# Optimization experiments

Hardware: AMD Instinct MI355X
Metric: run time of the kernel (lower is better)

The kernel has to match this reference:

```python
import jax, jax.numpy as jnp
import numpy as np

EPS = 1e-5
SLOPE = 0.01  # torch LeakyReLU default negative_slope


def _stage(h, W):
    # h: [B, N, k, Cin]; W: [Cout, Cin] (1x1 conv, no bias)
    h = jnp.einsum('bnkc,oc->bnko', h, W)
    # InstanceNorm2d (affine=False): normalize per (batch, channel) over spatial (N, k)
    mean = jnp.mean(h, axis=(1, 2), keepdims=True)
    var = jnp.var(h, axis=(1, 2), keepdims=True)
    h = (h - mean) * jax.lax.rsqrt(var + EPS)
    return jnp.where(h >= 0, h, SLOPE * h)


def setup_inputs() -> dict:
    key = jax.random.key(0)
    k1, k2, k3, k4, k5 = jax.random.split(key, 5)
    B, N, D, K, C = 8, 4096, 64, 20, 64
    x = jax.random.normal(k1, (B, N, D), dtype=jnp.float32)
    ind = jax.random.randint(k2, (B, N, K), 0, B * N, dtype=jnp.int64)
    W1 = jax.random.normal(k3, (C, 2 * D), dtype=jnp.float32) * 0.05
    W2 = jax.random.normal(k4, (C, C), dtype=jnp.float32) * 0.05
    W3 = jax.random.normal(k5, (C, C), dtype=jnp.float32) * 0.05
    return {"x": x, "ind": ind, "W1": W1, "W2": W2, "W3": W3}


def reference(x, ind, W1, W2, W3):
    B, N, D = x.shape
    k = ind.shape[2]
    # Gather neighbors via global (B*N) indices, as in the torch code
    y = x.reshape(B * N, D)[ind.reshape(B * N, k)].reshape(B, N, k, D)  # [B,N,k,D]
    xe = jnp.broadcast_to(x[:, :, None, :], (B, N, k, D))
    feat = jnp.concatenate([y - xe, xe], axis=3)  # [B,N,k,2D]
    h = _stage(feat, W1)
    h = _stage(h, W2)
    h = _stage(h, W3)
    # max-pool over k neighbors -> [B, N, Cout]
    return jnp.max(h, axis=2)
```

## Files before the change

kernel.cpp:

```cpp
#include <hip/hip_runtime.h>

#define BDIM 8
#define NPTS 4096
#define KNEI 20
#define BN (BDIM*NPTS)
#define NKCNT (NPTS*KNEI)
#define EPSI 1e-5f
#define SLOPE 0.01f

typedef _Float16 half_t;
typedef __attribute__((ext_vector_type(2))) _Float16 h2v;
typedef __attribute__((ext_vector_type(4))) _Float16 h4v;
typedef __attribute__((ext_vector_type(8))) _Float16 h8v;
typedef __attribute__((ext_vector_type(4))) float f32x4;
typedef __attribute__((ext_vector_type(2))) float f32x2;

__device__ __forceinline__ unsigned long long pack4_f16(const f32x4& a) {
    unsigned p0 = __builtin_bit_cast(unsigned, __builtin_amdgcn_cvt_pkrtz(a[0], a[1]));
    unsigned p1 = __builtin_bit_cast(unsigned, __builtin_amdgcn_cvt_pkrtz(a[2], a[3]));
    return ((unsigned long long)p1 << 32) | p0;
}

__global__ __launch_bounds__(256) void k0_uv(const float* __restrict__ x,
        const float* __restrict__ W1, const float* __restrict__ W2,
        const float* __restrict__ W3, half_t* __restrict__ u,
        half_t* __restrict__ v, half_t* __restrict__ Wh2,
        half_t* __restrict__ Wh3) {
    int tid = threadIdx.x;
    if (blockIdx.x >= BN / 16) {
        const float* src = (blockIdx.x == BN / 16) ? W2 : W3;
        half_t* dst = (blockIdx.x == BN / 16) ? Wh2 : Wh3;
        for (int i = tid; i < 4096; i += 256) dst[i] = (half_t)src[i];
        return;
    }
    __shared__ float wlds[64 * 129];
    __shared__ float xs[16 * 64];
    int m0 = blockIdx.x * 16;
    for (int i = tid; i < 8192; i += 256)
        wlds[(i >> 7) * 129 + (i & 127)] = W1[i];
    for (int i = tid; i < 1024; i += 256)
        xs[i] = x[m0 * 64 + i];
    __syncthreads();
    int o = tid & 63;
    int r0 = tid >> 6;
    float au[4] = {0.f, 0.f, 0.f, 0.f};
    float av[4] = {0.f, 0.f, 0.f, 0.f};
    for (int c = 0; c < 64; ++c) {
        float wa = wlds[o * 129 + c];
        float wb = wlds[o * 129 + 64 + c];
        float wd = wb - wa;
#pragma unroll
        for (int jj = 0; jj < 4; ++jj) {
            float xv = xs[(r0 + jj * 4) * 64 + c];
            au[jj] += xv * wa;
            av[jj] += xv * wd;
        }
    }
#pragma unroll
    for (int jj = 0; jj < 4; ++jj) {
        int m = m0 + r0 + jj * 4;
        u[(size_t)m * 64 + o] = (half_t)au[jj];
        v[(size_t)m * 64 + o] = (half_t)av[jj];
    }
}

__global__ __launch_bounds__(256) void k1_stats1(const half_t* __restrict__ u,
        const half_t* __restrict__ v, const int* __restrict__ ind,
        float* __restrict__ s1) {
    __shared__ float sacc[128];
    int tid = threadIdx.x;
    if (tid < 128) sacc[tid] = 0.f;
    int lane = tid & 63, w = tid >> 6;
    int b = blockIdx.x >> 8;
    int n0 = (blockIdx.x & 255) << 4;
    int p = b * NPTS + n0 + w * 4 + (lane >> 4);
    int c4 = lane & 15;
    h4v vv = *(const h4v*)(v + (size_t)p * 64 + c4 * 4);
    const int* ip = ind + (size_t)p * 20;
    float s0 = 0, s1v = 0, s2v = 0, s3v = 0, q0 = 0, q1 = 0, q2 = 0, q3 = 0;
#pragma unroll
    for (int r = 0; r < 20; ++r) {
        int idx = ip[r];
        h4v uu = *(const h4v*)(u + (size_t)idx * 64 + c4 * 4);
        h4v h = uu + vv;
        float f0 = h[0], f1 = h[1], f2 = h[2], f3 = h[3];
        s0 += f0; q0 = fmaf(f0, f0, q0);
        s1v += f1; q1 = fmaf(f1, f1, q1);
        s2v += f2; q2 = fmaf(f2, f2, q2);
        s3v += f3; q3 = fmaf(f3, f3, q3);
    }
    __syncthreads();
    atomicAdd(&sacc[c4 * 4 + 0], s0);  atomicAdd(&sacc[c4 * 4 + 1], s1v);
    atomicAdd(&sacc[c4 * 4 + 2], s2v); atomicAdd(&sacc[c4 * 4 + 3], s3v);
    atomicAdd(&sacc[64 + c4 * 4 + 0], q0); atomicAdd(&sacc[64 + c4 * 4 + 1], q1);
    atomicAdd(&sacc[64 + c4 * 4 + 2], q2); atomicAdd(&sacc[64 + c4 * 4 + 3], q3);
    __syncthreads();
    if (tid < 128)
        atomicAdd(&s1[(tid >> 6) * 512 + b * 64 + (tid & 63)], sacc[tid]);
}

__global__ __launch_bounds__(256, 3) void k2_stats2(const half_t* __restrict__ u,
        const half_t* __restrict__ v, const int* __restrict__ ind,
        const half_t* __restrict__ Wh2, const float* __restrict__ s1,
        float* __restrict__ s2) {
    __shared__ float sacc[128];
    int tid = threadIdx.x;
    if (tid < 128) sacc[tid] = 0.f;
    int lane = tid & 63, w = tid >> 6;
    int l15 = lane & 15, q = lane >> 4;
    int b = blockIdx.x >> 8;
    int n0 = (blockIdx.x & 255) << 4;
    int base = b * NPTS + n0;
    h8v aw[4][2];
#pragma unroll
    for (int mt = 0; mt < 4; ++mt)
#pragma unroll
        for (int kc = 0; kc < 2; ++kc)
            aw[mt][kc] = *(const h8v*)(Wh2 + (mt * 16 + l15) * 64 + kc * 32 + q * 8);
    const float inv = 1.0f / (float)NKCNT;
    h8v r1v[2], m1v[2];
#pragma unroll
    for (int kc = 0; kc < 2; ++kc)
#pragma unroll
        for (int j = 0; j < 8; ++j) {
            int c = kc * 32 + q * 8 + j;
            float mm = s1[b * 64 + c] * inv;
            float va = s1[512 + b * 64 + c] * inv - mm * mm;
            float rs = rsqrtf(va + EPSI);
            r1v[kc][j] = (half_t)rs;
            m1v[kc][j] = (half_t)(-mm * rs);
        }
    int idxs[5];
#pragma unroll
    for (int nt = 0; nt < 5; ++nt)
        idxs[nt] = ind[(size_t)base * 20 + w * 80 + nt * 16 + l15];
    float ss[4][4] = {}, sq[4][4] = {};
#pragma unroll
    for (int nt = 0; nt < 5; ++nt) {
        int row = w * 80 + nt * 16 + l15;
        int p = (row * 3277) >> 16;
        const half_t* up = u + (size_t)idxs[nt] * 64;
        const half_t* vp = v + (size_t)(base + p) * 64;
        h8v bfr[2];
#pragma unroll
        for (int kc = 0; kc < 2; ++kc) {
            h8v uu = *(const h8v*)(up + kc * 32 + q * 8);
            h8v vvv = *(const h8v*)(vp + kc * 32 + q * 8);
            h8v h = uu + vvv;
            h8v t = h * r1v[kc] + m1v[kc];
            bfr[kc] = __builtin_elementwise_max(t, t * (half_t)SLOPE);
        }
#pragma unroll
        for (int mt = 0; mt < 4; ++mt) {
            f32x4 a = {0.f, 0.f, 0.f, 0.f};
            a = __builtin_amdgcn_mfma_f32_16x16x32_f16(aw[mt][0], bfr[0], a, 0, 0, 0);
            a = __builtin_amdgcn_mfma_f32_16x16x32_f16(aw[mt][1], bfr[1], a, 0, 0, 0);
#pragma unroll
            for (int j = 0; j < 4; ++j) {
                ss[mt][j] += a[j];
                sq[mt][j] = fmaf(a[j], a[j], sq[mt][j]);
            }
        }
    }
#pragma unroll
    for (int m = 1; m < 16; m <<= 1)
#pragma unroll
        for (int mt = 0; mt < 4; ++mt)
#pragma unroll
            for (int j = 0; j < 4; ++j) {
                ss[mt][j] += __shfl_xor(ss[mt][j], m, 64);
                sq[mt][j] += __shfl_xor(sq[mt][j], m, 64);
            }
    __syncthreads();
    if (l15 == 0) {
#pragma unroll
        for (int mt = 0; mt < 4; ++mt)
#pragma unroll
            for (int j = 0; j < 4; ++j) {
                atomicAdd(&sacc[mt * 16 + q * 4 + j], ss[mt][j]);
                atomicAdd(&sacc[64 + mt * 16 + q * 4 + j], sq[mt][j]);
            }
    }
    __syncthreads();
    if (tid < 128)
        atomicAdd(&s2[(tid >> 6) * 512 + b * 64 + (tid & 63)], sacc[tid]);
}

__global__ __launch_bounds__(256, 3) void k3_fused(const half_t* __restrict__ u,
        const half_t* __restrict__ v, const int* __restrict__ ind,
        const half_t* __restrict__ Wh2, const half_t* __restrict__ Wh3,
        const float* __restrict__ s1, const float* __restrict__ s2,
        float* __restrict__ s3, float* __restrict__ out) {
    __shared__ __align__(16) unsigned char tile[40960];
    __shared__ float sacc[128];
    int tid = threadIdx.x;
    if (tid < 128) sacc[tid] = 0.f;
    int lane = tid & 63, w = tid >> 6;
    int l15 = lane & 15, q = lane >> 4;
    int b = blockIdx.x >> 8;
    int n0 = (blockIdx.x & 255) << 4;
    int base = b * NPTS + n0;
    const float inv = 1.0f / (float)NKCNT;
    h8v r1v[2], m1v[2], r2v[2], m2v[2];
#pragma unroll
    for (int kc = 0; kc < 2; ++kc)
#pragma unroll
        for (int j = 0; j < 8; ++j) {
            int c = kc * 32 + q * 8 + j;
            float mm = s1[b * 64 + c] * inv;
            float va = s1[512 + b * 64 + c] * inv - mm * mm;
            float rs = rsqrtf(va + EPSI);
            r1v[kc][j] = (half_t)rs;
            m1v[kc][j] = (half_t)(-mm * rs);
            float mm2 = s2[b * 64 + c] * inv;
            float va2 = s2[512 + b * 64 + c] * inv - mm2 * mm2;
            float rs2 = rsqrtf(va2 + EPSI);
            r2v[kc][j] = (half_t)rs2;
            m2v[kc][j] = (half_t)(-mm2 * rs2);
        }
    h8v aw[4][2];
#pragma unroll
    for (int mt = 0; mt < 4; ++mt)
#pragma unroll
        for (int kc = 0; kc < 2; ++kc)
            aw[mt][kc] = *(const h8v*)(Wh2 + (mt * 16 + l15) * 64 + kc * 32 + q * 8);
    int idxs[5];
#pragma unroll
    for (int nt = 0; nt < 5; ++nt)
        idxs[nt] = ind[(size_t)base * 20 + w * 80 + nt * 16 + l15];
#pragma unroll
    for (int nt = 0; nt < 5; ++nt) {
        int row = w * 80 + nt * 16 + l15;
        int p = (row * 3277) >> 16;
        int r7 = row & 7;
        const half_t* up = u + (size_t)idxs[nt] * 64;
        const half_t* vp = v + (size_t)(base + p) * 64;
        h8v bfr[2];
#pragma unroll
        for (int kc = 0; kc < 2; ++kc) {
            h8v uu = *(const h8v*)(up + kc * 32 + q * 8);
            h8v vvv = *(const h8v*)(vp + kc * 32 + q * 8);
            h8v h = uu + vvv;
            h8v t = h * r1v[kc] + m1v[kc];
            bfr[kc] = __builtin_elementwise_max(t, t * (half_t)SLOPE);
        }
#pragma unroll
        for (int mt = 0; mt < 4; ++mt) {
            f32x4 a = {0.f, 0.f, 0.f, 0.f};
            a = __builtin_amdgcn_mfma_f32_16x16x32_f16(aw[mt][0], bfr[0], a, 0, 0, 0);
            a = __builtin_amdgcn_mfma_f32_16x16x32_f16(aw[mt][1], bfr[1], a, 0, 0, 0);
            *(unsigned long long*)(tile + row * 128 +
                (((mt * 2 + (q >> 1)) ^ r7) << 4) + (q & 1) * 8) = pack4_f16(a);
        }
    }
    h8v bf2[5][2];
#pragma unroll
    for (int nt = 0; nt < 5; ++nt) {
        int row = w * 80 + nt * 16 + l15;
        int r7 = row & 7;
#pragma unroll
        for (int kc = 0; kc < 2; ++kc) {
            h8v hv = *(const h8v*)(tile + row * 128 + (((kc * 4 + q) ^ r7) << 4));
            h8v t = hv * r2v[kc] + m2v[kc];
            bf2[nt][kc] = __builtin_elementwise_max(t, t * (half_t)SLOPE);
        }
    }
    h8v aw3[4][2];
#pragma unroll
    for (int mt = 0; mt < 4; ++mt)
#pragma unroll
        for (int kc = 0; kc < 2; ++kc)
            aw3[mt][kc] = *(const h8v*)(Wh3 + (mt * 16 + l15) * 64 + kc * 32 + q * 8);
    float ss[4][4] = {}, sq[4][4] = {};
#pragma unroll
    for (int nt = 0; nt < 5; ++nt) {
        int row = w * 80 + nt * 16 + l15;
        int r7 = row & 7;
#pragma unroll
        for (int mt = 0; mt < 4; ++mt) {
            f32x4 a = {0.f, 0.f, 0.f, 0.f};
            a = __builtin_amdgcn_mfma_f32_16x16x32_f16(aw3[mt][0], bf2[nt][0], a, 0, 0, 0);
            a = __builtin_amdgcn_mfma_f32_16x16x32_f16(aw3[mt][1], bf2[nt][1], a, 0, 0, 0);
#pragma unroll
            for (int j = 0; j < 4; ++j) {
                ss[mt][j] += a[j];
                sq[mt][j] = fmaf(a[j], a[j], sq[mt][j]);
            }
            *(unsigned long long*)(tile + row * 128 +
                (((mt * 2 + (q >> 1)) ^ r7) << 4) + (q & 1) * 8) = pack4_f16(a);
        }
    }
#pragma unroll
    for (int m = 1; m < 16; m <<= 1)
#pragma unroll
        for (int mt = 0; mt < 4; ++mt)
#pragma unroll
            for (int j = 0; j < 4; ++j) {
                ss[mt][j] += __shfl_xor(ss[mt][j], m, 64);
                sq[mt][j] += __shfl_xor(sq[mt][j], m, 64);
            }
    __syncthreads();
    if (l15 == 0) {
#pragma unroll
        for (int mt = 0; mt < 4; ++mt)
#pragma unroll
            for (int j = 0; j < 4; ++j) {
                atomicAdd(&sacc[mt * 16 + q * 4 + j], ss[mt][j]);
                atomicAdd(&sacc[64 + mt * 16 + q * 4 + j], sq[mt][j]);
            }
    }
    {
        int c2 = tid & 31, g = tid >> 5;
#pragma unroll
        for (int pp = 0; pp < 2; ++pp) {
            int p = g * 2 + pp;
            h2v mx = {(half_t)-65504.f, (half_t)-65504.f};
            for (int kk = 0; kk < 20; ++kk) {
                int row = p * 20 + kk;
                unsigned hv = *(const unsigned*)(tile + row * 128 +
                    (((c2 >> 2) ^ (row & 7)) << 4) + (c2 & 3) * 4);
                mx = __builtin_elementwise_max(mx, __builtin_bit_cast(h2v, hv));
            }
            f32x2 o = {(float)mx[0], (float)mx[1]};
            *(f32x2*)(out + (size_t)(base + p) * 64 + c2 * 2) = o;
        }
    }
    __syncthreads();
    if (tid < 128)
        atomicAdd(&s3[(tid >> 6) * 512 + b * 64 + (tid & 63)], sacc[tid]);
}

__global__ __launch_bounds__(256) void k4_final(float* __restrict__ out,
        const float* __restrict__ s3) {
    int idx = blockIdx.x * 256 + threadIdx.x;
    int c = idx & 63;
    int b = idx >> 18;
    const float inv = 1.0f / (float)NKCNT;
    float mm = s3[b * 64 + c] * inv;
    float vv = s3[512 + b * 64 + c] * inv - mm * mm;
    float r = rsqrtf(vv + EPSI);
    float val = (out[idx] - mm) * r;
    out[idx] = val >= 0.f ? val : SLOPE * val;
}

extern "C" void kernel_launch(void* const* d_in, const int* in_sizes, int n_in,
                              void* d_out, int out_size, void* d_ws, size_t ws_size,
                              hipStream_t stream) {
    const float* x   = (const float*)d_in[0];
    const int*   ind = (const int*)d_in[1];
    const float* W1  = (const float*)d_in[2];
    const float* W2  = (const float*)d_in[3];
    const float* W3  = (const float*)d_in[4];
    float* out = (float*)d_out;

    half_t* u   = (half_t*)d_ws;
    half_t* v   = u + (size_t)BN * 64;
    half_t* Wh2 = v + (size_t)BN * 64;
    half_t* Wh3 = Wh2 + 4096;
    float* stats = (float*)(Wh3 + 4096);
    float* s1 = stats;
    float* s2 = stats + 1024;
    float* s3 = stats + 2048;

    (void)hipMemsetAsync(stats, 0, 3 * 1024 * sizeof(float), stream);
    k0_uv<<<dim3(BN / 16 + 2), dim3(256), 0, stream>>>(x, W1, W2, W3, u, v, Wh2, Wh3);
    k1_stats1<<<dim3(BN / 16), dim3(256), 0, stream>>>(u, v, ind, s1);
    k2_stats2<<<dim3(BN / 16), dim3(256), 0, stream>>>(u, v, ind, Wh2, s1, s2);
    k3_fused<<<dim3(BN / 16), dim3(256), 0, stream>>>(u, v, ind, Wh2, Wh3, s1, s2, s3, out);
    k4_final<<<dim3(BN * 64 / 256), dim3(256), 0, stream>>>(out, s3);
}
```

Before: 207.8 us.

## Remap neighbor rows per point, stage weights in LDS, max-pool in registers

The MFMA column mapping changes so each group of lanes handles the 20 neighbors of one point. The center-point v row is then loaded once per lane instead of per neighbor, and the k-max pool is done in registers with shuffles instead of through a 40KB LDS tile. Weights for stages 2 and 3 move into swizzled LDS, and a small per-wave scratch replaces the big tile. This cuts LDS and registers so occupancy can rise to 4 blocks/SM. k1_stats1 also switches to 8-wide loads with a shuffle reduction to cut LDS atomics. The cost is extra LDS weight reads inside the MFMA loops.

```diff
diff --git a/kernel.cpp b/kernel.cpp
--- a/kernel.cpp
+++ b/kernel.cpp
@@ -15,9 +15,12 @@
 typedef __attribute__((ext_vector_type(4))) float f32x4;
 typedef __attribute__((ext_vector_type(2))) float f32x2;
 
+__device__ __forceinline__ h2v cvt2(float a, float b) {
+    return __builtin_bit_cast(h2v, __builtin_amdgcn_cvt_pkrtz(a, b));
+}
 __device__ __forceinline__ unsigned long long pack4_f16(const f32x4& a) {
-    unsigned p0 = __builtin_bit_cast(unsigned, __builtin_amdgcn_cvt_pkrtz(a[0], a[1]));
-    unsigned p1 = __builtin_bit_cast(unsigned, __builtin_amdgcn_cvt_pkrtz(a[2], a[3]));
+    unsigned p0 = __builtin_bit_cast(unsigned, cvt2(a[0], a[1]));
+    unsigned p1 = __builtin_bit_cast(unsigned, cvt2(a[2], a[3]));
     return ((unsigned long long)p1 << 32) | p0;
 }
 
@@ -74,32 +77,42 @@
     int b = blockIdx.x >> 8;
     int n0 = (blockIdx.x & 255) << 4;
     int p = b * NPTS + n0 + w * 4 + (lane >> 4);
-    int c4 = lane & 15;
-    h4v vv = *(const h4v*)(v + (size_t)p * 64 + c4 * 4);
+    int rh = (lane >> 3) & 1, c8 = lane & 7;
+    h8v vv = *(const h8v*)(v + (size_t)p * 64 + c8 * 8);
     const int* ip = ind + (size_t)p * 20;
-    float s0 = 0, s1v = 0, s2v = 0, s3v = 0, q0 = 0, q1 = 0, q2 = 0, q3 = 0;
-#pragma unroll
-    for (int r = 0; r < 20; ++r) {
-        int idx = ip[r];
-        h4v uu = *(const h4v*)(u + (size_t)idx * 64 + c4 * 4);
-        h4v h = uu + vv;
-        float f0 = h[0], f1 = h[1], f2 = h[2], f3 = h[3];
-        s0 += f0; q0 = fmaf(f0, f0, q0);
-        s1v += f1; q1 = fmaf(f1, f1, q1);
-        s2v += f2; q2 = fmaf(f2, f2, q2);
-        s3v += f3; q3 = fmaf(f3, f3, q3);
-    }
-    __syncthreads();
-    atomicAdd(&sacc[c4 * 4 + 0], s0);  atomicAdd(&sacc[c4 * 4 + 1], s1v);
-    atomicAdd(&sacc[c4 * 4 + 2], s2v); atomicAdd(&sacc[c4 * 4 + 3], s3v);
-    atomicAdd(&sacc[64 + c4 * 4 + 0], q0); atomicAdd(&sacc[64 + c4 * 4 + 1], q1);
-    atomicAdd(&sacc[64 + c4 * 4 + 2], q2); atomicAdd(&sacc[64 + c4 * 4 + 3], q3);
+    float s[8] = {}, qa[8] = {};
+#pragma unroll
+    for (int r = 0; r < 10; ++r) {
+        int idx = ip[r * 2 + rh];
+        h8v uu = *(const h8v*)(u + (size_t)idx * 64 + c8 * 8);
+        h8v h = uu + vv;
+#pragma unroll
+        for (int j = 0; j < 8; ++j) {
+            float f = (float)h[j];
+            s[j] += f; qa[j] = fmaf(f, f, qa[j]);
+        }
+    }
+#pragma unroll
+    for (int m = 8; m <= 32; m <<= 1)
+#pragma unroll
+        for (int j = 0; j < 8; ++j) {
+            s[j] += __shfl_xor(s[j], m, 64);
+            qa[j] += __shfl_xor(qa[j], m, 64);
+        }
+    __syncthreads();
+    if ((lane & 56) == 0) {
+#pragma unroll
+        for (int j = 0; j < 8; ++j) {
+            atomicAdd(&sacc[c8 * 8 + j], s[j]);
+            atomicAdd(&sacc[64 + c8 * 8 + j], qa[j]);
+        }
+    }
     __syncthreads();
     if (tid < 128)
         atomicAdd(&s1[(tid >> 6) * 512 + b * 64 + (tid & 63)], sacc[tid]);
 }
 
-__global__ __launch_bounds__(256, 3) void k2_stats2(const half_t* __restrict__ u,
+__global__ __launch_bounds__(256, 4) void k2_stats2(const half_t* __restrict__ u,
         const half_t* __restrict__ v, const int* __restrict__ ind,
         const half_t* __restrict__ Wh2, const float* __restrict__ s1,
         float* __restrict__ s2) {
@@ -111,6 +124,7 @@
     int b = blockIdx.x >> 8;
     int n0 = (blockIdx.x & 255) << 4;
     int base = b * NPTS + n0;
+    int base20 = base * 20;
     h8v aw[4][2];
 #pragma unroll
     for (int mt = 0; mt < 4; ++mt)
@@ -130,23 +144,24 @@
             r1v[kc][j] = (half_t)rs;
             m1v[kc][j] = (half_t)(-mm * rs);
         }
+    int gp = base + w * 4 + (l15 >> 2);
+    h8v vfr[2];
+#pragma unroll
+    for (int kc = 0; kc < 2; ++kc)
+        vfr[kc] = *(const h8v*)(v + (size_t)gp * 64 + kc * 32 + q * 8);
     int idxs[5];
 #pragma unroll
     for (int nt = 0; nt < 5; ++nt)
-        idxs[nt] = ind[(size_t)base * 20 + w * 80 + nt * 16 + l15];
+        idxs[nt] = ind[base20 + w * 80 + l15 * 5 + nt];
     float ss[4][4] = {}, sq[4][4] = {};
 #pragma unroll
     for (int nt = 0; nt < 5; ++nt) {
-        int row = w * 80 + nt * 16 + l15;
-        int p = (row * 3277) >> 16;
         const half_t* up = u + (size_t)idxs[nt] * 64;
-        const half_t* vp = v + (size_t)(base + p) * 64;
         h8v bfr[2];
 #pragma unroll
         for (int kc = 0; kc < 2; ++kc) {
             h8v uu = *(const h8v*)(up + kc * 32 + q * 8);
-            h8v vvv = *(const h8v*)(vp + kc * 32 + q * 8);
-            h8v h = uu + vvv;
+            h8v h = uu + vfr[kc];
             h8v t = h * r1v[kc] + m1v[kc];
             bfr[kc] = __builtin_elementwise_max(t, t * (half_t)SLOPE);
         }
@@ -186,20 +201,30 @@
         atomicAdd(&s2[(tid >> 6) * 512 + b * 64 + (tid & 63)], sacc[tid]);
 }
 
-__global__ __launch_bounds__(256, 3) void k3_fused(const half_t* __restrict__ u,
+__global__ __launch_bounds__(256, 4) void k3_fused(const half_t* __restrict__ u,
         const half_t* __restrict__ v, const int* __restrict__ ind,
         const half_t* __restrict__ Wh2, const half_t* __restrict__ Wh3,
         const float* __restrict__ s1, const float* __restrict__ s2,
         float* __restrict__ s3, float* __restrict__ out) {
-    __shared__ __align__(16) unsigned char tile[40960];
+    __shared__ __align__(16) unsigned char wlds[16384];
+    __shared__ __align__(16) unsigned char scr[16384];
     __shared__ float sacc[128];
     int tid = threadIdx.x;
     if (tid < 128) sacc[tid] = 0.f;
     int lane = tid & 63, w = tid >> 6;
     int l15 = lane & 15, q = lane >> 4;
+    int rw7 = l15 & 7;
     int b = blockIdx.x >> 8;
     int n0 = (blockIdx.x & 255) << 4;
     int base = b * NPTS + n0;
+    int base20 = base * 20;
+    for (int i = tid; i < 512; i += 256) {
+        int rw = i >> 3, ch = i & 7;
+        *(h8v*)(wlds + rw * 128 + ((ch ^ (rw & 7)) << 4)) =
+            *(const h8v*)(Wh2 + rw * 64 + ch * 8);
+        *(h8v*)(wlds + 8192 + rw * 128 + ((ch ^ (rw & 7)) << 4)) =
+            *(const h8v*)(Wh3 + rw * 64 + ch * 8);
+    }
     const float inv = 1.0f / (float)NKCNT;
     h8v r1v[2], m1v[2], r2v[2], m2v[2];
 #pragma unroll
@@ -218,77 +243,89 @@
             r2v[kc][j] = (half_t)rs2;
             m2v[kc][j] = (half_t)(-mm2 * rs2);
         }
-    h8v aw[4][2];
-#pragma unroll
-    for (int mt = 0; mt < 4; ++mt)
-#pragma unroll
-        for (int kc = 0; kc < 2; ++kc)
-            aw[mt][kc] = *(const h8v*)(Wh2 + (mt * 16 + l15) * 64 + kc * 32 + q * 8);
+    int gp = base + w * 4 + (l15 >> 2);
+    h8v vfr[2];
+#pragma unroll
+    for (int kc = 0; kc < 2; ++kc)
+        vfr[kc] = *(const h8v*)(v + (size_t)gp * 64 + kc * 32 + q * 8);
     int idxs[5];
 #pragma unroll
     for (int nt = 0; nt < 5; ++nt)
-        idxs[nt] = ind[(size_t)base * 20 + w * 80 + nt * 16 + l15];
+        idxs[nt] = ind[base20 + w * 80 + l15 * 5 + nt];
+    __syncthreads();
+    h8v bf2[5][2];
 #pragma unroll
     for (int nt = 0; nt < 5; ++nt) {
-        int row = w * 80 + nt * 16 + l15;
-        int p = (row * 3277) >> 16;
-        int r7 = row & 7;
+        unsigned char* scrw = scr + w * 4096 + (nt & 1) * 2048;
         const half_t* up = u + (size_t)idxs[nt] * 64;
-        const half_t* vp = v + (size_t)(base + p) * 64;
         h8v bfr[2];
 #pragma unroll
         for (int kc = 0; kc < 2; ++kc) {
             h8v uu = *(const h8v*)(up + kc * 32 + q * 8);
-            h8v vvv = *(const h8v*)(vp + kc * 32 + q * 8);
-            h8v h = uu + vvv;
+            h8v h = uu + vfr[kc];
             h8v t = h * r1v[kc] + m1v[kc];
             bfr[kc] = __builtin_elementwise_max(t, t * (half_t)SLOPE);
         }
 #pragma unroll
         for (int mt = 0; mt < 4; ++mt) {
+            h8v w0 = *(const h8v*)(wlds + (mt * 16 + l15) * 128 + ((q ^ rw7) << 4));
+            h8v w1 = *(const h8v*)(wlds + (mt * 16 + l15) * 128 + (((4 + q) ^ rw7) << 4));
             f32x4 a = {0.f, 0.f, 0.f, 0.f};
-            a = __builtin_amdgcn_mfma_f32_16x16x32_f16(aw[mt][0], bfr[0], a, 0, 0, 0);
-            a = __builtin_amdgcn_mfma_f32_16x16x32_f16(aw[mt][1], bfr[1], a, 0, 0, 0);
-            *(unsigned long long*)(tile + row * 128 +
-                (((mt * 2 + (q >> 1)) ^ r7) << 4) + (q & 1) * 8) = pack4_f16(a);
-        }
-    }
-    h8v bf2[5][2];
-#pragma unroll
-    for (int nt = 0; nt < 5; ++nt) {
-        int row = w * 80 + nt * 16 + l15;
-        int r7 = row & 7;
+            a = __builtin_amdgcn_mfma_f32_16x16x32_f16(w0, bfr[0], a, 0, 0, 0);
+            a = __builtin_amdgcn_mfma_f32_16x16x32_f16(w1, bfr[1], a, 0, 0, 0);
+            *(unsigned long long*)(scrw + l15 * 128 +
+                (((mt * 2 + (q >> 1)) ^ rw7) << 4) + (q & 1) * 8) = pack4_f16(a);
+        }
 #pragma unroll
         for (int kc = 0; kc < 2; ++kc) {
-            h8v hv = *(const h8v*)(tile + row * 128 + (((kc * 4 + q) ^ r7) << 4));
+            h8v hv = *(const h8v*)(scrw + l15 * 128 + (((kc * 4 + q) ^ rw7) << 4));
             h8v t = hv * r2v[kc] + m2v[kc];
             bf2[nt][kc] = __builtin_elementwise_max(t, t * (half_t)SLOPE);
         }
     }
-    h8v aw3[4][2];
+    float ss[4][4] = {}, sq[4][4] = {};
+    h2v pm[4][2];
 #pragma unroll
     for (int mt = 0; mt < 4; ++mt)
 #pragma unroll
-        for (int kc = 0; kc < 2; ++kc)
-            aw3[mt][kc] = *(const h8v*)(Wh3 + (mt * 16 + l15) * 64 + kc * 32 + q * 8);
-    float ss[4][4] = {}, sq[4][4] = {};
+        for (int r = 0; r < 2; ++r)
+            pm[mt][r] = (h2v){(half_t)-65504.f, (half_t)-65504.f};
 #pragma unroll
     for (int nt = 0; nt < 5; ++nt) {
-        int row = w * 80 + nt * 16 + l15;
-        int r7 = row & 7;
 #pragma unroll
         for (int mt = 0; mt < 4; ++mt) {
+            h8v w0 = *(const h8v*)(wlds + 8192 + (mt * 16 + l15) * 128 + ((q ^ rw7) << 4));
+            h8v w1 = *(const h8v*)(wlds + 8192 + (mt * 16 + l15) * 128 + (((4 + q) ^ rw7) << 4));
             f32x4 a = {0.f, 0.f, 0.f, 0.f};
-            a = __builtin_amdgcn_mfma_f32_16x16x32_f16(aw3[mt][0], bf2[nt][0], a, 0, 0, 0);
-            a = __builtin_amdgcn_mfma_f32_16x16x32_f16(aw3[mt][1], bf2[nt][1], a, 0, 0, 0);
+            a = __builtin_amdgcn_mfma_f32_16x16x32_f16(w0, bf2[nt][0], a, 0, 0, 0);
+            a = __builtin_amdgcn_mfma_f32_16x16x32_f16(w1, bf2[nt][1], a, 0, 0, 0);
 #pragma unroll
             for (int j = 0; j < 4; ++j) {
                 ss[mt][j] += a[j];
                 sq[mt][j] = fmaf(a[j], a[j], sq[mt][j]);
             }
-            *(unsigned long long*)(tile + row * 128 +
-                (((mt * 2 + (q >> 1)) ^ r7) << 4) + (q & 1) * 8) = pack4_f16(a);
-        }
+            h2v p0 = cvt2(a[0], a[1]);
+            h2v p1 = cvt2(a[2], a[3]);
+            pm[mt][0] = __builtin_elementwise_max(pm[mt][0], p0);
+            pm[mt][1] = __builtin_elementwise_max(pm[mt][1], p1);
+        }
+    }
+#pragma unroll
+    for (int m = 1; m <= 2; m <<= 1)
+#pragma unroll
+        for (int mt = 0; mt < 4; ++mt)
+#pragma unroll
+            for (int r = 0; r < 2; ++r) {
+                int t = __shfl_xor(__builtin_bit_cast(int, pm[mt][r]), m, 64);
+                pm[mt][r] = __builtin_elementwise_max(pm[mt][r],
+                               __builtin_bit_cast(h2v, t));
+            }
+    {
+        int ms = l15 & 3;
+        h2v sa = ms == 0 ? pm[0][0] : ms == 1 ? pm[1][0] : ms == 2 ? pm[2][0] : pm[3][0];
+        h2v sb = ms == 0 ? pm[0][1] : ms == 1 ? pm[1][1] : ms == 2 ? pm[2][1] : pm[3][1];
+        f32x4 o = {(float)sa[0], (float)sa[1], (float)sb[0], (float)sb[1]};
+        *(f32x4*)(out + (size_t)gp * 64 + ms * 16 + q * 4) = o;
     }
 #pragma unroll
     for (int m = 1; m < 16; m <<= 1)
@@ -299,7 +336,6 @@
                 ss[mt][j] += __shfl_xor(ss[mt][j], m, 64);
                 sq[mt][j] += __shfl_xor(sq[mt][j], m, 64);
             }
-    __syncthreads();
     if (l15 == 0) {
 #pragma unroll
         for (int mt = 0; mt < 4; ++mt)
@@ -308,22 +344,6 @@
                 atomicAdd(&sacc[mt * 16 + q * 4 + j], ss[mt][j]);
                 atomicAdd(&sacc[64 + mt * 16 + q * 4 + j], sq[mt][j]);
             }
-    }
-    {
-        int c2 = tid & 31, g = tid >> 5;
-#pragma unroll
-        for (int pp = 0; pp < 2; ++pp) {
-            int p = g * 2 + pp;
-            h2v mx = {(half_t)-65504.f, (half_t)-65504.f};
-            for (int kk = 0; kk < 20; ++kk) {
-                int row = p * 20 + kk;
-                unsigned hv = *(const unsigned*)(tile + row * 128 +
-                    (((c2 >> 2) ^ (row & 7)) << 4) + (c2 & 3) * 4);
-                mx = __builtin_elementwise_max(mx, __builtin_bit_cast(h2v, hv));
-            }
-            f32x2 o = {(float)mx[0], (float)mx[1]};
-            *(f32x2*)(out + (size_t)(base + p) * 64 + c2 * 2) = o;
-        }
     }
     __syncthreads();
     if (tid < 128)
```

Measured after the change: 185.6 us. -10.7%, faster.
